# Performance work log

Measured on AMD Instinct MI355X. Metric: run time of the kernel, lower is better.

Reference implementation:

```python
import jax, jax.numpy as jnp
import numpy as np

M, K, D = 64, 32, 32   # antennas, users, hidden features
PT = 1.0               # total transmit power
BS = 1024


def _glorot(key, shape):
    fan_out, fan_in = shape
    lim = np.sqrt(6.0 / (fan_in + fan_out)).astype(np.float32)
    return jax.random.uniform(key, shape, minval=-lim, maxval=lim, dtype=jnp.float32)


def setup_inputs() -> dict:
    key = jax.random.key(0)
    ks = jax.random.split(key, 16)
    inp = {"x": jax.random.normal(ks[0], (BS, M, K, 2), dtype=jnp.float32)}
    dims = [(D, 2), (D, D), (D, D), (D, D), (2, D)]
    i = 1
    for l, sh in enumerate(dims, start=1):
        for tag in ("s", "m", "k"):
            inp[f"W{l}{tag}"] = _glorot(ks[i], sh)
            i += 1
    return inp


def gnn_layer(x, Ws, Wm, Wk):
    # x: (b, M, K, d_in); weights: (d_out, d_in)
    msg_m = jnp.sum(x, axis=2)  # (b, M, d_in) aggregate over users per antenna
    msg_k = jnp.sum(x, axis=1)  # (b, K, d_in) aggregate over antennas per user
    z = (jnp.einsum('hd,bmkd->bmkh', Ws, x)
         + jnp.einsum('hd,bmd->bmh', Wm, msg_m)[:, :, None, :]
         + jnp.einsum('hd,bkd->bkh', Wk, msg_k)[:, None, :, :])
    return z  # (b, M, K, d_out)


def pwr_norm(x):
    # x: (b, M, K, 2) -> |W|_F^2 = sum over m,k of re^2+im^2
    power = jnp.sum(x * x, axis=(1, 2, 3), keepdims=True)
    alpha = jnp.sqrt(PT / power)
    return alpha * x


def reference(x, W1s, W1m, W1k, W2s, W2m, W2k, W3s, W3m, W3k,
              W4s, W4m, W4k, W5s, W5m, W5k):
    h = jax.nn.relu(gnn_layer(x, W1s, W1m, W1k))
    h = jax.nn.relu(gnn_layer(h, W2s, W2m, W2k))
    h = jax.nn.relu(gnn_layer(h, W3s, W3m, W3k))
    h = jax.nn.relu(gnn_layer(h, W4s, W4m, W4k))
    h = gnn_layer(h, W5s, W5m, W5k)
    return pwr_norm(h)
```

## Files before the change

### kernel.cpp

```cpp
#include <hip/hip_runtime.h>
#include <hip/hip_fp16.h>


namespace {

constexpr int NTHREADS = 1024;
constexpr float INPUT_SCALE = 0.0625f;
constexpr float LAYER_SCALE = 0.0078125f;
constexpr int XPLANE = 16384;

typedef _Float16 half8 __attribute__((ext_vector_type(8)));
typedef _Float16 half2v __attribute__((ext_vector_type(2)));
typedef float    f32x4 __attribute__((ext_vector_type(4)));
typedef unsigned uint4v __attribute__((ext_vector_type(4)));

#define RPT32(X) X(0)X(1)X(2)X(3)X(4)X(5)X(6)X(7)X(8)X(9)X(10)X(11)X(12)X(13)X(14)X(15) \
                 X(16)X(17)X(18)X(19)X(20)X(21)X(22)X(23)X(24)X(25)X(26)X(27)X(28)X(29)X(30)X(31)
#define RPT16P(X) X(0,0,1)X(1,2,3)X(2,4,5)X(3,6,7)X(4,8,9)X(5,10,11)X(6,12,13)X(7,14,15) \
                  X(8,16,17)X(9,18,19)X(10,20,21)X(11,22,23)X(12,24,25)X(13,26,27)X(14,28,29)X(15,30,31)

#define AB_OFF(h) ((((h) >> 2) & 3) * 8 + (((h) >> 4) & 1) * 4 + ((h) & 3))

__device__ __forceinline__ float2 upk(unsigned w) {
    __half2 h;
    *reinterpret_cast<unsigned*>(&h) = w;
    return __half22float2(h);
}
__device__ __forceinline__ unsigned pkz(float a, float b) {
    auto h = __builtin_amdgcn_cvt_pkrtz(a, b);
    return __builtin_bit_cast(unsigned, h);
}
__device__ __forceinline__ unsigned hadd2u(unsigned a, unsigned b) {
    half2v x = __builtin_bit_cast(half2v, a);
    half2v y = __builtin_bit_cast(half2v, b);
    return __builtin_bit_cast(unsigned, x + y);
}
__device__ __forceinline__ unsigned hmax0u(unsigned a) {
    unsigned r;
    asm("v_pk_max_f16 %0, %1, 0" : "=v"(r) : "v"(a));
    return r;
}
template <int CTRL>
__device__ __forceinline__ uint4v dpp_hadd(uint4v s) {
    uint4v r;
    r.x = hadd2u(s.x, (unsigned)__builtin_amdgcn_mov_dpp((int)s.x, CTRL, 0xF, 0xF, true));
    r.y = hadd2u(s.y, (unsigned)__builtin_amdgcn_mov_dpp((int)s.y, CTRL, 0xF, 0xF, true));
    r.z = hadd2u(s.z, (unsigned)__builtin_amdgcn_mov_dpp((int)s.z, CTRL, 0xF, 0xF, true));
    r.w = hadd2u(s.w, (unsigned)__builtin_amdgcn_mov_dpp((int)s.w, CTRL, 0xF, 0xF, true));
    return r;
}

__device__ __forceinline__ half8 load_wfrag(const float* __restrict__ W, int h, int quad,
                                            float scale) {
    const float4* wr = reinterpret_cast<const float4*>(W + h * 32 + quad * 8);
    const float4 w0 = wr[0];
    const float4 w1 = wr[1];
    half8 b;
    b[0] = (_Float16)(w0.x * scale); b[1] = (_Float16)(w0.y * scale);
    b[2] = (_Float16)(w0.z * scale); b[3] = (_Float16)(w0.w * scale);
    b[4] = (_Float16)(w1.x * scale); b[5] = (_Float16)(w1.y * scale);
    b[6] = (_Float16)(w1.z * scale); b[7] = (_Float16)(w1.w * scale);
    return b;
}

__device__ __forceinline__ void phase_msg(const unsigned* __restrict__ Xs,
                                          unsigned* __restrict__ MSG, int t) {
    if (t < 512) {
        const int k = t >> 4, fq = (t >> 2) & 3, mq = t & 3;
        const unsigned* p = Xs + (fq >> 1) * XPLANE + mq * 4096 + k * 8 + (fq & 1) * 4;
        half8 accA{}, accB{};
#pragma unroll
        for (int i = 0; i < 16; i += 2) {
            accA += __builtin_bit_cast(half8, *(const uint4v*)(p + i * 256));
            accB += __builtin_bit_cast(half8, *(const uint4v*)(p + (i + 1) * 256));
        }
        uint4v s = __builtin_bit_cast(uint4v, accA + accB);
        s = dpp_hadd<0xB1>(s);
        s = dpp_hadd<0x4E>(s);
        if (mq == 0) *(uint4v*)(MSG + (64 + k) * 20 + fq * 4) = s;
    } else {
        const int u = t - 512;
        const int m = u >> 3, fq = (u >> 1) & 3, kh = u & 1;
        const unsigned* base = Xs + (fq >> 1) * XPLANE + m * 256 + kh * 128 + (fq & 1) * 4;
        const unsigned rot = (unsigned)((m & 15) * 8);
        half8 accA{}, accB{};
#pragma unroll
        for (int i = 0; i < 16; i += 2) {
            accA += __builtin_bit_cast(half8, *(const uint4v*)(base + (((unsigned)(i * 8)) ^ rot)));
            accB += __builtin_bit_cast(half8, *(const uint4v*)(base + (((unsigned)((i + 1) * 8)) ^ rot)));
        }
        uint4v s = __builtin_bit_cast(uint4v, accA + accB);
        s = dpp_hadd<0xB1>(s);
        if (kh == 0) *(uint4v*)(MSG + m * 20 + fq * 4) = s;
    }
}

__device__ __forceinline__ void phase_small(const float* __restrict__ Wmg,
                                            const float* __restrict__ Wkg,
                                            const unsigned* __restrict__ MSG,
                                            unsigned* __restrict__ ABu, int t) {
    const int w = t >> 6, lane = t & 63;
    if (w < 12) {
        const int isb = (w >= 8);
        const int ww = isb ? (w - 8) : w;
        const int nt = ww >> 1, ht = ww & 1;
        const int quad = lane >> 4, col = lane & 15;
        const int rowbase = (isb ? 64 : 0) + nt * 16;
        const uint4v mraw = *(const uint4v*)(MSG + (rowbase + col) * 20 + quad * 4);
        const half8 bfrag = __builtin_bit_cast(half8, mraw);
        const half8 afrag = load_wfrag(isb ? Wkg : Wmg, ht * 16 + col, quad, LAYER_SCALE);
        f32x4 c = {0.f, 0.f, 0.f, 0.f};
        c = __builtin_amdgcn_mfma_f32_16x16x32_f16(afrag, bfrag, c, 0, 0, 0);
        uint2 st;
        st.x = pkz(c[0], c[1]);
        st.y = pkz(c[2], c[3]);
        *reinterpret_cast<uint2*>(ABu + (rowbase + col) * 20 + quad * 4 + ht * 2) = st;
    }
}

__device__ __forceinline__ void phase_main(const float* __restrict__ Wsg,
                                           unsigned* __restrict__ Xs,
                                           const unsigned* __restrict__ ABu, int t) {
    const int w = t >> 6, lane = t & 63;
    const int quad = lane >> 4, col = lane & 15;
    const half8 a0 = load_wfrag(Wsg, col, quad, LAYER_SCALE);
    const half8 a1 = load_wfrag(Wsg, 16 + col, quad, LAYER_SCALE);
    const uint4v* AB4 = reinterpret_cast<const uint4v*>(ABu);
    const unsigned* xr = Xs + (quad >> 1) * XPLANE + col * 8 + (quad & 1) * 4;
    unsigned* xw = Xs + col * 8 + quad * 2;
#pragma unroll 2
    for (int i = 0; i < 8; ++i) {
        const int T = w + i * 16;
        const int node0 = T * 16;
        const int m = T >> 1;
        const int k0 = (T & 1) * 16;
        const half8 b = __builtin_bit_cast(half8, *(const uint4v*)(xr + node0 * 8));
        const int krow = 64 + k0 + col;
        const uint4v Am = AB4[m * 5 + quad];
        const uint4v Bk = AB4[krow * 5 + quad];
        const float2 p00 = upk(hadd2u(Am.x, Bk.x));
        const float2 p01 = upk(hadd2u(Am.y, Bk.y));
        const float2 p10 = upk(hadd2u(Am.z, Bk.z));
        const float2 p11 = upk(hadd2u(Am.w, Bk.w));
        f32x4 c0 = {p00.x, p00.y, p01.x, p01.y};
        f32x4 c1 = {p10.x, p10.y, p11.x, p11.y};
        c0 = __builtin_amdgcn_mfma_f32_16x16x32_f16(a0, b, c0, 0, 0, 0);
        c1 = __builtin_amdgcn_mfma_f32_16x16x32_f16(a1, b, c1, 0, 0, 0);
        uint2 w0, w1;
        w0.x = hmax0u(pkz(c0[0], c0[1]));
        w0.y = hmax0u(pkz(c0[2], c0[3]));
        w1.x = hmax0u(pkz(c1[0], c1[1]));
        w1.y = hmax0u(pkz(c1[2], c1[3]));
        *reinterpret_cast<uint2*>(xw + node0 * 8) = w0;
        *reinterpret_cast<uint2*>(xw + node0 * 8 + XPLANE) = w1;
    }
}

__global__ void __launch_bounds__(NTHREADS) gnn_fused(
    const float* __restrict__ xg,
    const float* __restrict__ w1s, const float* __restrict__ w1m, const float* __restrict__ w1k,
    const float* __restrict__ w2s, const float* __restrict__ w2m, const float* __restrict__ w2k,
    const float* __restrict__ w3s, const float* __restrict__ w3m, const float* __restrict__ w3k,
    const float* __restrict__ w4s, const float* __restrict__ w4m, const float* __restrict__ w4k,
    const float* __restrict__ w5s, const float* __restrict__ w5m, const float* __restrict__ w5k,
    float* __restrict__ out)
{
    __shared__ __align__(16) unsigned Xs[2 * XPLANE];
    __shared__ __align__(16) unsigned MSG[96 * 20];
    __shared__ __align__(16) unsigned ABu[96 * 20];
    __shared__ float red[17];

    const int t = threadIdx.x;
    const int b = blockIdx.x;
    const int k = t & 31;
    const int m1 = t >> 5;
    const int m2 = m1 + 32;
    const int lane = t & 63;
    const int wave = t >> 6;

    float2 a1 = *reinterpret_cast<const float2*>(xg + (size_t)b * 4096 + 2 * t);
    float2 a2 = *reinterpret_cast<const float2*>(xg + (size_t)b * 4096 + 2048 + 2 * t);
    a1.x *= INPUT_SCALE; a1.y *= INPUT_SCALE;
    a2.x *= INPUT_SCALE; a2.y *= INPUT_SCALE;

    _Float16* ABf = reinterpret_cast<_Float16*>(ABu);
    float* MSGf = reinterpret_cast<float*>(MSG);

    if (t < 64) MSGf[t] = 0.f;
    __syncthreads();
    {
        float s0 = a1.x + a2.x, s1 = a1.y + a2.y;
        s0 += __shfl_xor(s0, 32);
        s1 += __shfl_xor(s1, 32);
        if (lane < 32) {
            atomicAdd(&MSGf[2 * k], s0);
            atomicAdd(&MSGf[2 * k + 1], s1);
        }
        float f0 = a1.x, f1 = a1.y, g0 = a2.x, g1 = a2.y;
#pragma unroll
        for (int mask = 1; mask <= 16; mask <<= 1) {
            f0 += __shfl_xor(f0, mask); f1 += __shfl_xor(f1, mask);
            g0 += __shfl_xor(g0, mask); g1 += __shfl_xor(g1, mask);
        }
        const float2 wm = *reinterpret_cast<const float2*>(w1m + 2 * k);
        ABf[m1 * 40 + AB_OFF(k)] = (_Float16)(wm.x * f0 + wm.y * f1);
        ABf[m2 * 40 + AB_OFF(k)] = (_Float16)(wm.x * g0 + wm.y * g1);
    }
    __syncthreads();
    {
        const int kk = t >> 5, hh = t & 31;
        const float2 wk2 = *reinterpret_cast<const float2*>(w1k + 2 * hh);
        ABf[(64 + kk) * 40 + AB_OFF(hh)] =
            (_Float16)(wk2.x * MSGf[2 * kk] + wk2.y * MSGf[2 * kk + 1]);
    }
    __syncthreads();
#pragma unroll 1
    for (int hf = 0; hf < 2; ++hf) {
        const int n = hf ? (t + 1024) : t;
        const int m = hf ? m2 : m1;
        const float xa = hf ? a2.x : a1.x;
        const float xb = hf ? a2.y : a1.y;
#define DECL_ACC(h) float acc##h = (float)ABf[m * 40 + AB_OFF(h)] \
                                 + (float)ABf[(64 + k) * 40 + AB_OFF(h)] \
                                 + w1s[h * 2] * xa + w1s[h * 2 + 1] * xb;
        RPT32(DECL_ACC)
#undef DECL_ACC
        unsigned tmp[16];
#define ST(p, h0, h1) tmp[p] = pkz(fmaxf(acc##h0, 0.f) * LAYER_SCALE, \
                                   fmaxf(acc##h1, 0.f) * LAYER_SCALE);
        RPT16P(ST)
#undef ST
        unsigned* xd = Xs + n * 8;
        uint4v v0, v1, v2, v3;
        v0.x = tmp[0];  v0.y = tmp[1];  v0.z = tmp[2];  v0.w = tmp[3];
        v1.x = tmp[4];  v1.y = tmp[5];  v1.z = tmp[6];  v1.w = tmp[7];
        v2.x = tmp[8];  v2.y = tmp[9];  v2.z = tmp[10]; v2.w = tmp[11];
        v3.x = tmp[12]; v3.y = tmp[13]; v3.z = tmp[14]; v3.w = tmp[15];
        *reinterpret_cast<uint4v*>(xd) = v0;
        *reinterpret_cast<uint4v*>(xd + 4) = v1;
        *reinterpret_cast<uint4v*>(xd + XPLANE) = v2;
        *reinterpret_cast<uint4v*>(xd + XPLANE + 4) = v3;
    }
    __syncthreads();

    phase_msg(Xs, MSG, t); __syncthreads();
    phase_small(w2m, w2k, MSG, ABu, t); __syncthreads();
    phase_main(w2s, Xs, ABu, t); __syncthreads();

    phase_msg(Xs, MSG, t); __syncthreads();
    phase_small(w3m, w3k, MSG, ABu, t); __syncthreads();
    phase_main(w3s, Xs, ABu, t); __syncthreads();

    phase_msg(Xs, MSG, t); __syncthreads();
    phase_small(w4m, w4k, MSG, ABu, t); __syncthreads();
    phase_main(w4s, Xs, ABu, t); __syncthreads();

    phase_msg(Xs, MSG, t); __syncthreads();
    if (t < 128) {
        const int m = t & 63, h = t >> 6;
        float acc = 0.f;
#pragma unroll
        for (int p = 0; p < 16; ++p) {
            const float2 u = upk(MSG[m * 20 + p]);
            acc += w5m[h * 32 + 2 * p] * u.x + w5m[h * 32 + 2 * p + 1] * u.y;
        }
        ABf[m * 40 + h] = (_Float16)acc;
    } else if (t < 192) {
        const int idx = t - 128;
        const int kk = idx & 31, h = idx >> 5;
        float acc = 0.f;
#pragma unroll
        for (int p = 0; p < 16; ++p) {
            const float2 u = upk(MSG[(64 + kk) * 20 + p]);
            acc += w5k[h * 32 + 2 * p] * u.x + w5k[h * 32 + 2 * p + 1] * u.y;
        }
        ABf[(64 + kk) * 40 + h] = (_Float16)acc;
    }
    __syncthreads();

    float za0 = (float)ABf[m1 * 40 + 0] + (float)ABf[(64 + k) * 40 + 0];
    float za1 = (float)ABf[m1 * 40 + 1] + (float)ABf[(64 + k) * 40 + 1];
    float zb0 = (float)ABf[m2 * 40 + 0] + (float)ABf[(64 + k) * 40 + 0];
    float zb1 = (float)ABf[m2 * 40 + 1] + (float)ABf[(64 + k) * 40 + 1];
    {
        const unsigned* xa0 = Xs + t * 8;
        const unsigned* xb0 = Xs + (t + 1024) * 8;
#pragma unroll
        for (int p = 0; p < 16; ++p) {
            const unsigned ua = (p < 8) ? xa0[p] : xa0[XPLANE + (p - 8)];
            const float2 u = upk(ua);
            za0 += w5s[2 * p] * u.x + w5s[2 * p + 1] * u.y;
            za1 += w5s[32 + 2 * p] * u.x + w5s[32 + 2 * p + 1] * u.y;
            const unsigned ub = (p < 8) ? xb0[p] : xb0[XPLANE + (p - 8)];
            const float2 v = upk(ub);
            zb0 += w5s[2 * p] * v.x + w5s[2 * p + 1] * v.y;
            zb1 += w5s[32 + 2 * p] * v.x + w5s[32 + 2 * p + 1] * v.y;
        }
    }

    float p2 = za0 * za0 + za1 * za1 + zb0 * zb0 + zb1 * zb1;
#pragma unroll
    for (int mask = 1; mask <= 32; mask <<= 1) p2 += __shfl_xor(p2, mask);
    if (lane == 0) red[wave] = p2;
    __syncthreads();
    if (t == 0) {
        float tot = 0.f;
#pragma unroll
        for (int i = 0; i < 16; ++i) tot += red[i];
        red[16] = rsqrtf(tot);
    }
    __syncthreads();
    const float alpha = red[16];

    float2 r1, r2;
    r1.x = alpha * za0; r1.y = alpha * za1;
    r2.x = alpha * zb0; r2.y = alpha * zb1;
    *reinterpret_cast<float2*>(out + (size_t)b * 4096 + 2 * t) = r1;
    *reinterpret_cast<float2*>(out + (size_t)b * 4096 + 2048 + 2 * t) = r2;
}

}

extern "C" void kernel_launch(void* const* d_in, const int* in_sizes, int n_in,
                              void* d_out, int out_size, void* d_ws, size_t ws_size,
                              hipStream_t stream) {
    const float* xg  = (const float*)d_in[0];
    const float* w1s = (const float*)d_in[1];
    const float* w1m = (const float*)d_in[2];
    const float* w1k = (const float*)d_in[3];
    const float* w2s = (const float*)d_in[4];
    const float* w2m = (const float*)d_in[5];
    const float* w2k = (const float*)d_in[6];
    const float* w3s = (const float*)d_in[7];
    const float* w3m = (const float*)d_in[8];
    const float* w3k = (const float*)d_in[9];
    const float* w4s = (const float*)d_in[10];
    const float* w4m = (const float*)d_in[11];
    const float* w4k = (const float*)d_in[12];
    const float* w5s = (const float*)d_in[13];
    const float* w5m = (const float*)d_in[14];
    const float* w5k = (const float*)d_in[15];
    float* out = (float*)d_out;

    hipLaunchKernelGGL(gnn_fused, dim3(1024), dim3(NTHREADS), 0, stream,
                       xg, w1s, w1m, w1k, w2s, w2m, w2k, w3s, w3m, w3k,
                       w4s, w4m, w4k, w5s, w5m, w5k, out);
}
```

Measured before the change: 209.5 us.

## Interleave feature halves per node with XOR swizzle and split message reductions

Changes the shared-memory activation layout from two separate feature planes to one 64-byte row per node, with XOR swizzling of 16-byte chunks to avoid bank conflicts. The main MFMA phase now does a single 128-bit load and a single 128-bit store per node instead of split-plane accesses. The message aggregation is remapped to all waves, writing partial sums (2 partials per antenna, 4 per user) that the small-GEMM phase folds via accumulated MFMAs, and the weight fragment load order is permuted to match. This adds MSG shared memory and extra MFMAs in exchange for fewer bank conflicts and more balanced reduction work.

```diff
diff --git a/kernel.cpp b/kernel.cpp
--- a/kernel.cpp
+++ b/kernel.cpp
@@ -7,7 +7,6 @@
 constexpr int NTHREADS = 1024;
 constexpr float INPUT_SCALE = 0.0625f;
 constexpr float LAYER_SCALE = 0.0078125f;
-constexpr int XPLANE = 16384;
 
 typedef _Float16 half8 __attribute__((ext_vector_type(8)));
 typedef _Float16 half2v __attribute__((ext_vector_type(2)));
@@ -20,6 +19,7 @@
                   X(8,16,17)X(9,18,19)X(10,20,21)X(11,22,23)X(12,24,25)X(13,26,27)X(14,28,29)X(15,30,31)
 
 #define AB_OFF(h) ((((h) >> 2) & 3) * 8 + (((h) >> 4) & 1) * 4 + ((h) & 3))
+#define PSLOT(s) (2 * ((s) >> 2) + 8 * (((s) >> 1) & 1) + ((s) & 1))
 
 __device__ __forceinline__ float2 upk(unsigned w) {
     __half2 h;
@@ -52,9 +52,8 @@
 
 __device__ __forceinline__ half8 load_wfrag(const float* __restrict__ W, int h, int quad,
                                             float scale) {
-    const float4* wr = reinterpret_cast<const float4*>(W + h * 32 + quad * 8);
-    const float4 w0 = wr[0];
-    const float4 w1 = wr[1];
+    const float4 w0 = *reinterpret_cast<const float4*>(W + h * 32 + quad * 4);
+    const float4 w1 = *reinterpret_cast<const float4*>(W + h * 32 + 16 + quad * 4);
     half8 b;
     b[0] = (_Float16)(w0.x * scale); b[1] = (_Float16)(w0.y * scale);
     b[2] = (_Float16)(w0.z * scale); b[3] = (_Float16)(w0.w * scale);
@@ -65,33 +64,46 @@
 
 __device__ __forceinline__ void phase_msg(const unsigned* __restrict__ Xs,
                                           unsigned* __restrict__ MSG, int t) {
-    if (t < 512) {
-        const int k = t >> 4, fq = (t >> 2) & 3, mq = t & 3;
-        const unsigned* p = Xs + (fq >> 1) * XPLANE + mq * 4096 + k * 8 + (fq & 1) * 4;
+    const int l = t & 63, w = t >> 6;
+    {
+        const int k3 = l & 7;
+        const int k = ((w & 3) << 3) | k3;
+        const int chunk = w >> 2;
+        const int mo = l >> 3;
+        const int chunkp = chunk ^ ((k3 >> 1) & 3);
+        const unsigned* p = Xs + mo * 4096 + k * 16 + chunkp * 4;
+        half8 acc{};
+#pragma unroll
+        for (int j = 0; j < 8; ++j)
+            acc += __builtin_bit_cast(half8, *(const uint4v*)(p + j * 512));
+        uint4v s = __builtin_bit_cast(uint4v, acc);
+        s = dpp_hadd<0x128>(s);
+        if ((l & 8) == 0) {
+            const int qi = l >> 4;
+            *(uint4v*)(MSG + (128 + qi * 32 + k) * 20 + chunk * 4) = s;
+        }
+    }
+    {
+        const int k3 = l & 7;
+        const int chunk = (l >> 3) & 3;
+        const int mlow = ((l >> 5) & 1) | ((w & 15) << 1);
+        const int chunkp = chunk ^ ((k3 >> 1) & 3);
+        const unsigned* p = Xs + mlow * 512 + k3 * 16 + chunkp * 4;
         half8 accA{}, accB{};
 #pragma unroll
-        for (int i = 0; i < 16; i += 2) {
-            accA += __builtin_bit_cast(half8, *(const uint4v*)(p + i * 256));
-            accB += __builtin_bit_cast(half8, *(const uint4v*)(p + (i + 1) * 256));
-        }
-        uint4v s = __builtin_bit_cast(uint4v, accA + accB);
-        s = dpp_hadd<0xB1>(s);
-        s = dpp_hadd<0x4E>(s);
-        if (mq == 0) *(uint4v*)(MSG + (64 + k) * 20 + fq * 4) = s;
-    } else {
-        const int u = t - 512;
-        const int m = u >> 3, fq = (u >> 1) & 3, kh = u & 1;
-        const unsigned* base = Xs + (fq >> 1) * XPLANE + m * 256 + kh * 128 + (fq & 1) * 4;
-        const unsigned rot = (unsigned)((m & 15) * 8);
-        half8 accA{}, accB{};
-#pragma unroll
-        for (int i = 0; i < 16; i += 2) {
-            accA += __builtin_bit_cast(half8, *(const uint4v*)(base + (((unsigned)(i * 8)) ^ rot)));
-            accB += __builtin_bit_cast(half8, *(const uint4v*)(base + (((unsigned)((i + 1) * 8)) ^ rot)));
-        }
-        uint4v s = __builtin_bit_cast(uint4v, accA + accB);
-        s = dpp_hadd<0xB1>(s);
-        if (kh == 0) *(uint4v*)(MSG + m * 20 + fq * 4) = s;
+        for (int j = 0; j < 4; ++j) {
+            accA += __builtin_bit_cast(half8, *(const uint4v*)(p + j * 128));
+            accB += __builtin_bit_cast(half8, *(const uint4v*)(p + 16384 + j * 128));
+        }
+        uint4v sA = __builtin_bit_cast(uint4v, accA);
+        uint4v sB = __builtin_bit_cast(uint4v, accB);
+        sA = dpp_hadd<0xB1>(sA); sA = dpp_hadd<0x4E>(sA);
+        sB = dpp_hadd<0xB1>(sB); sB = dpp_hadd<0x4E>(sB);
+        if ((l & 3) == 0) {
+            const int set = (l >> 2) & 1;
+            *(uint4v*)(MSG + (mlow + set * 64) * 20 + chunk * 4) = sA;
+            *(uint4v*)(MSG + (mlow + 32 + set * 64) * 20 + chunk * 4) = sB;
+        }
     }
 }
 
@@ -105,16 +117,30 @@
         const int ww = isb ? (w - 8) : w;
         const int nt = ww >> 1, ht = ww & 1;
         const int quad = lane >> 4, col = lane & 15;
-        const int rowbase = (isb ? 64 : 0) + nt * 16;
-        const uint4v mraw = *(const uint4v*)(MSG + (rowbase + col) * 20 + quad * 4);
-        const half8 bfrag = __builtin_bit_cast(half8, mraw);
         const half8 afrag = load_wfrag(isb ? Wkg : Wmg, ht * 16 + col, quad, LAYER_SCALE);
         f32x4 c = {0.f, 0.f, 0.f, 0.f};
-        c = __builtin_amdgcn_mfma_f32_16x16x32_f16(afrag, bfrag, c, 0, 0, 0);
+        if (isb) {
+            const int r0 = 128 + nt * 16 + col;
+#pragma unroll
+            for (int s = 0; s < 4; ++s) {
+                const half8 bf = __builtin_bit_cast(half8,
+                    *(const uint4v*)(MSG + (r0 + s * 32) * 20 + quad * 4));
+                c = __builtin_amdgcn_mfma_f32_16x16x32_f16(afrag, bf, c, 0, 0, 0);
+            }
+        } else {
+            const int r0 = nt * 16 + col;
+#pragma unroll
+            for (int s = 0; s < 2; ++s) {
+                const half8 bf = __builtin_bit_cast(half8,
+                    *(const uint4v*)(MSG + (r0 + s * 64) * 20 + quad * 4));
+                c = __builtin_amdgcn_mfma_f32_16x16x32_f16(afrag, bf, c, 0, 0, 0);
+            }
+        }
         uint2 st;
         st.x = pkz(c[0], c[1]);
         st.y = pkz(c[2], c[3]);
-        *reinterpret_cast<uint2*>(ABu + (rowbase + col) * 20 + quad * 4 + ht * 2) = st;
+        const int abrow = (isb ? 64 : 0) + nt * 16 + col;
+        *reinterpret_cast<uint2*>(ABu + abrow * 20 + quad * 4 + ht * 2) = st;
     }
 }
 
@@ -126,15 +152,14 @@
     const half8 a0 = load_wfrag(Wsg, col, quad, LAYER_SCALE);
     const half8 a1 = load_wfrag(Wsg, 16 + col, quad, LAYER_SCALE);
     const uint4v* AB4 = reinterpret_cast<const uint4v*>(ABu);
-    const unsigned* xr = Xs + (quad >> 1) * XPLANE + col * 8 + (quad & 1) * 4;
-    unsigned* xw = Xs + col * 8 + quad * 2;
+    unsigned* xp = Xs + col * 16 + ((quad ^ ((col >> 1) & 3)) << 2);
 #pragma unroll 2
     for (int i = 0; i < 8; ++i) {
         const int T = w + i * 16;
-        const int node0 = T * 16;
         const int m = T >> 1;
-        const int k0 = (T & 1) * 16;
-        const half8 b = __builtin_bit_cast(half8, *(const uint4v*)(xr + node0 * 8));
+        const int k0 = (T & 1) << 4;
+        unsigned* xc = xp + T * 256;
+        const half8 b = __builtin_bit_cast(half8, *(const uint4v*)xc);
         const int krow = 64 + k0 + col;
         const uint4v Am = AB4[m * 5 + quad];
         const uint4v Bk = AB4[krow * 5 + quad];
@@ -146,13 +171,12 @@
         f32x4 c1 = {p10.x, p10.y, p11.x, p11.y};
         c0 = __builtin_amdgcn_mfma_f32_16x16x32_f16(a0, b, c0, 0, 0, 0);
         c1 = __builtin_amdgcn_mfma_f32_16x16x32_f16(a1, b, c1, 0, 0, 0);
-        uint2 w0, w1;
-        w0.x = hmax0u(pkz(c0[0], c0[1]));
-        w0.y = hmax0u(pkz(c0[2], c0[3]));
-        w1.x = hmax0u(pkz(c1[0], c1[1]));
-        w1.y = hmax0u(pkz(c1[2], c1[3]));
-        *reinterpret_cast<uint2*>(xw + node0 * 8) = w0;
-        *reinterpret_cast<uint2*>(xw + node0 * 8 + XPLANE) = w1;
+        uint4v st;
+        st.x = hmax0u(pkz(c0[0], c0[1]));
+        st.y = hmax0u(pkz(c0[2], c0[3]));
+        st.z = hmax0u(pkz(c1[0], c1[1]));
+        st.w = hmax0u(pkz(c1[2], c1[3]));
+        *(uint4v*)xc = st;
     }
 }
 
@@ -165,8 +189,8 @@
     const float* __restrict__ w5s, const float* __restrict__ w5m, const float* __restrict__ w5k,
     float* __restrict__ out)
 {
-    __shared__ __align__(16) unsigned Xs[2 * XPLANE];
-    __shared__ __align__(16) unsigned MSG[96 * 20];
+    __shared__ __align__(16) unsigned Xs[2048 * 16];
+    __shared__ __align__(16) unsigned MSG[256 * 20];
     __shared__ __align__(16) unsigned ABu[96 * 20];
     __shared__ float red[17];
 
@@ -177,6 +201,7 @@
     const int m2 = m1 + 32;
     const int lane = t & 63;
     const int wave = t >> 6;
+    const int sw1 = (t >> 1) & 3;
 
     float2 a1 = *reinterpret_cast<const float2*>(xg + (size_t)b * 4096 + 2 * t);
     float2 a2 = *reinterpret_cast<const float2*>(xg + (size_t)b * 4096 + 2048 + 2 * t);
@@ -230,16 +255,16 @@
                                    fmaxf(acc##h1, 0.f) * LAYER_SCALE);
         RPT16P(ST)
 #undef ST
-        unsigned* xd = Xs + n * 8;
+        unsigned* xd = Xs + n * 16;
         uint4v v0, v1, v2, v3;
-        v0.x = tmp[0];  v0.y = tmp[1];  v0.z = tmp[2];  v0.w = tmp[3];
-        v1.x = tmp[4];  v1.y = tmp[5];  v1.z = tmp[6];  v1.w = tmp[7];
-        v2.x = tmp[8];  v2.y = tmp[9];  v2.z = tmp[10]; v2.w = tmp[11];
-        v3.x = tmp[12]; v3.y = tmp[13]; v3.z = tmp[14]; v3.w = tmp[15];
-        *reinterpret_cast<uint4v*>(xd) = v0;
-        *reinterpret_cast<uint4v*>(xd + 4) = v1;
-        *reinterpret_cast<uint4v*>(xd + XPLANE) = v2;
-        *reinterpret_cast<uint4v*>(xd + XPLANE + 4) = v3;
+        v0.x = tmp[0]; v0.y = tmp[1]; v0.z = tmp[8];  v0.w = tmp[9];
+        v1.x = tmp[2]; v1.y = tmp[3]; v1.z = tmp[10]; v1.w = tmp[11];
+        v2.x = tmp[4]; v2.y = tmp[5]; v2.z = tmp[12]; v2.w = tmp[13];
+        v3.x = tmp[6]; v3.y = tmp[7]; v3.z = tmp[14]; v3.w = tmp[15];
+        *(uint4v*)(xd + ((0 ^ sw1) << 2)) = v0;
+        *(uint4v*)(xd + ((1 ^ sw1) << 2)) = v1;
+        *(uint4v*)(xd + ((2 ^ sw1) << 2)) = v2;
+        *(uint4v*)(xd + ((3 ^ sw1) << 2)) = v3;
     }
     __syncthreads();
 
@@ -260,9 +285,12 @@
         const int m = t & 63, h = t >> 6;
         float acc = 0.f;
 #pragma unroll
-        for (int p = 0; p < 16; ++p) {
-            const float2 u = upk(MSG[m * 20 + p]);
-            acc += w5m[h * 32 + 2 * p] * u.x + w5m[h * 32 + 2 * p + 1] * u.y;
+        for (int s = 0; s < 16; ++s) {
+            const int pp = PSLOT(s);
+            const float2 uA = upk(MSG[m * 20 + s]);
+            const float2 uB = upk(MSG[(64 + m) * 20 + s]);
+            acc += w5m[h * 32 + 2 * pp] * (uA.x + uB.x)
+                 + w5m[h * 32 + 2 * pp + 1] * (uA.y + uB.y);
         }
         ABf[m * 40 + h] = (_Float16)acc;
     } else if (t < 192) {
@@ -270,9 +298,15 @@
         const int kk = idx & 31, h = idx >> 5;
         float acc = 0.f;
 #pragma unroll
-        for (int p = 0; p < 16; ++p) {
-            const float2 u = upk(MSG[(64 + kk) * 20 + p]);
-            acc += w5k[h * 32 + 2 * p] * u.x + w5k[h * 32 + 2 * p + 1] * u.y;
+        for (int s = 0; s < 16; ++s) {
+            const int pp = PSLOT(s);
+            float ux = 0.f, uy = 0.f;
+#pragma unroll
+            for (int qq = 0; qq < 4; ++qq) {
+                const float2 u = upk(MSG[(128 + qq * 32 + kk) * 20 + s]);
+                ux += u.x; uy += u.y;
+            }
+            acc += w5k[h * 32 + 2 * pp] * ux + w5k[h * 32 + 2 * pp + 1] * uy;
         }
         ABf[(64 + kk) * 40 + h] = (_Float16)acc;
     }
@@ -283,18 +317,18 @@
     float zb0 = (float)ABf[m2 * 40 + 0] + (float)ABf[(64 + k) * 40 + 0];
     float zb1 = (float)ABf[m2 * 40 + 1] + (float)ABf[(64 + k) * 40 + 1];
     {
-        const unsigned* xa0 = Xs + t * 8;
-        const unsigned* xb0 = Xs + (t + 1024) * 8;
-#pragma unroll
-        for (int p = 0; p < 16; ++p) {
-            const unsigned ua = (p < 8) ? xa0[p] : xa0[XPLANE + (p - 8)];
-            const float2 u = upk(ua);
-            za0 += w5s[2 * p] * u.x + w5s[2 * p + 1] * u.y;
-            za1 += w5s[32 + 2 * p] * u.x + w5s[32 + 2 * p + 1] * u.y;
-            const unsigned ub = (p < 8) ? xb0[p] : xb0[XPLANE + (p - 8)];
-            const float2 v = upk(ub);
-            zb0 += w5s[2 * p] * v.x + w5s[2 * p + 1] * v.y;
-            zb1 += w5s[32 + 2 * p] * v.x + w5s[32 + 2 * p + 1] * v.y;
+        const unsigned* xa0 = Xs + t * 16;
+        const unsigned* xb0 = xa0 + 16384;
+#pragma unroll
+        for (int s = 0; s < 16; ++s) {
+            const int idx = ((((s >> 2) ^ sw1) << 2)) | (s & 3);
+            const int pp = PSLOT(s);
+            const float2 u = upk(xa0[idx]);
+            za0 += w5s[2 * pp] * u.x + w5s[2 * pp + 1] * u.y;
+            za1 += w5s[32 + 2 * pp] * u.x + w5s[32 + 2 * pp + 1] * u.y;
+            const float2 v = upk(xb0[idx]);
+            zb0 += w5s[2 * pp] * v.x + w5s[2 * pp + 1] * v.y;
+            zb1 += w5s[32 + 2 * pp] * v.x + w5s[32 + 2 * pp + 1] * v.y;
         }
     }
 
```

Result: faster. 203.4 us (-2.9%).
